# Kernel tuning notes

Hardware: AMD Instinct MI355X
Metric: run time of the kernel (lower is better)

The kernel has to match this reference:

```python
import jax, jax.numpy as jnp
import numpy as np


def setup_inputs() -> dict:
    key = jax.random.key(0)
    k1, k2, k3 = jax.random.split(key, 3)
    bs, chart_len, H = 256, 1024, 256
    num_steps, start_index = 512, 512
    chart = jax.random.normal(k1, (bs, chart_len, 2 * H), dtype=jnp.float32)
    operations = jax.random.randint(k2, (num_steps, bs, 2), 0, start_index, dtype=jnp.int64)
    U = jax.random.normal(k3, (5 * H, 2 * H), dtype=jnp.float32) * 0.05
    b = jnp.zeros((5 * H,), dtype=jnp.float32)
    return {"chart": chart, "operations": operations, "start_index": start_index, "U": U, "b": b}


def reference(chart, operations, start_index, U, b):
    H = U.shape[0] // 5
    bs = chart.shape[0]
    batch_idx = jnp.arange(bs)
    num_steps = operations.shape[0]

    def step_fn(ch, xs):
        step, ops = xs
        left = ch[batch_idx, ops[:, 0]]   # [bs, 2H]
        right = ch[batch_idx, ops[:, 1]]  # [bs, 2H]
        ccL, ccR = left[:, :H], right[:, :H]
        hh = jnp.concatenate([left[:, H:], right[:, H:]], axis=-1)  # [bs, 2H]
        preact = hh @ U.T + b  # [bs, 5H]
        i = jax.nn.sigmoid(preact[:, :H])
        fL = jax.nn.sigmoid(preact[:, H:2 * H])
        fR = jax.nn.sigmoid(preact[:, 2 * H:3 * H])
        o = jax.nn.sigmoid(preact[:, 3 * H:4 * H])
        u = jnp.tanh(preact[:, 4 * H:5 * H])
        c = fL * ccL + fR * ccR + i * u
        h = o * jnp.tanh(c)
        ch = ch.at[:, start_index + step, :].set(jnp.concatenate([c, h], axis=-1))
        return ch, None

    chart, _ = jax.lax.scan(step_fn, chart, (jnp.arange(num_steps), operations))
    return chart
```

## Files before the change

kernel.cpp:

```cpp
#include <hip/hip_runtime.h>
#include <hip/hip_bf16.h>

#define H_     256
#define TWOH_  512
#define CL_    1024
#define BS_    256
#define START_ 512

typedef float  f32x16   __attribute__((ext_vector_type(16)));
typedef short  short8_t __attribute__((ext_vector_type(8)));
typedef short  short4_t __attribute__((ext_vector_type(4)));
typedef __bf16 bf16x8   __attribute__((ext_vector_type(8)));

static __device__ __forceinline__ unsigned short f2bf(float x) {
  __hip_bfloat16 h = __float2bfloat16(x);
  return __builtin_bit_cast(unsigned short, h);
}

static __device__ __forceinline__ void gload16(const void* g, void* l) {
  __builtin_amdgcn_global_load_lds(
      (const __attribute__((address_space(1))) void*)g,
      (__attribute__((address_space(3))) void*)l, 16, 0, 0);
}

#define SCHED0() __builtin_amdgcn_sched_barrier(0)

__global__ void uconv_kernel(const float* __restrict__ U,
                             unsigned short* __restrict__ ub) {
  int tid = blockIdx.x * 256 + threadIdx.x;
  if (tid >= 1280 * 512) return;
  int n = tid >> 9, k = tid & 511;
  int g = n >> 8, j = n & 255;
  int jc = j >> 6, c = (g << 6) + (j & 63);
  ub[((jc * 320 + c) << 9) + k] = f2bf(U[tid]);
}

__global__ void hbconv_kernel(const float* __restrict__ chart,
                              unsigned short* __restrict__ hb) {
  size_t t = (size_t)blockIdx.x * 256 + threadIdx.x;
  size_t row = t >> 5;
  int    kc  = (int)(t & 31) * 8;
  size_t i = row >> 9, pos = row & 511;
  const float* src = chart + (i * CL_ + pos) * TWOH_ + H_ + kc;
  float4 f0 = *(const float4*)(src);
  float4 f1 = *(const float4*)(src + 4);
  short8_t v;
  v[0] = (short)f2bf(f0.x); v[1] = (short)f2bf(f0.y);
  v[2] = (short)f2bf(f0.z); v[3] = (short)f2bf(f0.w);
  v[4] = (short)f2bf(f1.x); v[5] = (short)f2bf(f1.y);
  v[6] = (short)f2bf(f1.z); v[7] = (short)f2bf(f1.w);
  *(short8_t*)(hb + row * H_ + kc) = v;
}

__global__ void copy_kernel(const float4* __restrict__ src,
                            float4* __restrict__ dst) {
  long long tid = (long long)blockIdx.x * blockDim.x + threadIdx.x;
  const long long total = 16777216LL;
  for (long long e = tid; e < total; e += (long long)gridDim.x * blockDim.x) {
    long long i   = e >> 16;
    long long rem = e & 65535;
    long long off = (i << 17) + rem;
    dst[off] = src[off];
  }
}

__global__ __launch_bounds__(256, 2) void chart3_kernel(
    const float* __restrict__ chart,
    const int* __restrict__ ops,
    const unsigned short* __restrict__ ub,
    const unsigned short* __restrict__ hb,
    const float* __restrict__ bias,
    float* __restrict__ out)
{
  __shared__ unsigned short As[2][128 * 32];
  __shared__ unsigned short Bs[2][320 * 32];
  __shared__ int opsl[256];

  const int tid = threadIdx.x;
  const int bx  = blockIdx.x;
  const int q5  = bx / 5;
  const int r5  = bx - q5 * 5;

  if (r5 == 4) {
    const float4* src = (const float4*)chart;
    float4* dst = (float4*)out;
    const long long base = (long long)q5 * 16384 + tid;
    #pragma unroll 4
    for (int it = 0; it < 64; ++it) {
      long long e   = base + it * 256;
      long long i   = e >> 16;
      long long rem = e & 65535;
      long long off = (i << 17) + rem;
      dst[off] = src[off];
    }
    return;
  }

  const int lane = tid & 63, wid = tid >> 6;
  const int l31 = lane & 31, lhi = lane >> 5;
  const int wm = wid & 1, wn = wid >> 1;
  const int s = q5 >> 1, ibase = (q5 & 1) * 128, jc = r5;

  opsl[tid] = ops[(s * BS_ + ibase) * 2 + tid];

  int rA[2], opAL[2], opAR[2], csA[2];
  #pragma unroll
  for (int q = 0; q < 2; ++q) {
    rA[q]   = (wid * 2 + q) * 16 + (lane >> 2);
    opAL[q] = ops[(s * BS_ + ibase + rA[q]) * 2];
    opAR[q] = ops[(s * BS_ + ibase + rA[q]) * 2 + 1];
    csA[q]  = (((lane & 3) ^ ((rA[q] >> 1) & 3))) * 8;
  }
  int rB[5], csB[5];
  #pragma unroll
  for (int p = 0; p < 5; ++p) {
    rB[p]  = (wid * 5 + p) * 16 + (lane >> 2);
    csB[p] = (((lane & 3) ^ ((rB[p] >> 1) & 3))) * 8;
  }
  const size_t ub_base = ((size_t)jc * 320) << 9;

  f32x16 acc0[5], acc1[5];
  #pragma unroll
  for (int g = 0; g < 5; ++g)
    #pragma unroll
    for (int q = 0; q < 16; ++q) { acc0[g][q] = 0.f; acc1[g][q] = 0.f; }

#define STAGE(BUF, KT) do {                                                     \
    const int  kt_   = (KT);                                                    \
    const bool left_ = kt_ < 8;                                                 \
    const int  koff_ = left_ ? kt_ * 32 : kt_ * 32 - 256;                       \
    _Pragma("unroll")                                                           \
    for (int q = 0; q < 2; ++q) {                                               \
      int op_ = left_ ? opAL[q] : opAR[q];                                      \
      const unsigned short* g_ =                                                \
          hb + ((size_t)(ibase + rA[q]) * 512 + op_) * 256 + koff_ + csA[q];    \
      gload16(g_, &As[BUF][(wid * 2 + q) * 512]);                               \
    }                                                                           \
    _Pragma("unroll")                                                           \
    for (int p = 0; p < 5; ++p) {                                               \
      const unsigned short* g_ =                                                \
          ub + ub_base + ((size_t)rB[p] << 9) + kt_ * 32 + csB[p];              \
      gload16(g_, &Bs[BUF][(wid * 5 + p) * 512]);                               \
    }                                                                           \
  } while (0)

  const int sw   = (l31 >> 1) & 3;
  const int aro0 = (wm * 64 + l31) * 32;
  const int aro1 = (wm * 64 + 32 + l31) * 32;
  const int bro  = (wn * 32 + l31) * 32;

#define COMPUTE(BUF) do {                                                       \
    _Pragma("unroll")                                                           \
    for (int ks = 0; ks < 2; ++ks) {                                            \
      const int ce = ((ks * 2 + lhi) ^ sw) * 8;                                 \
      bf16x8 a0 = __builtin_bit_cast(bf16x8,                                    \
          *(const short8_t*)&As[BUF][aro0 + ce]);                               \
      bf16x8 a1 = __builtin_bit_cast(bf16x8,                                    \
          *(const short8_t*)&As[BUF][aro1 + ce]);                               \
      _Pragma("unroll")                                                         \
      for (int g = 0; g < 5; ++g) {                                             \
        bf16x8 b = __builtin_bit_cast(bf16x8,                                   \
            *(const short8_t*)&Bs[BUF][bro + g * 2048 + ce]);                   \
        acc0[g] = __builtin_amdgcn_mfma_f32_32x32x16_bf16(a0, b, acc0[g],0,0,0);\
        acc1[g] = __builtin_amdgcn_mfma_f32_32x32x16_bf16(a1, b, acc1[g],0,0,0);\
      }                                                                         \
    }                                                                           \
  } while (0)

#define PHASE(BUF, KT, DOSTAGE) do {                                            \
    asm volatile("s_waitcnt vmcnt(7)" ::: "memory");                            \
    __builtin_amdgcn_s_barrier();                                               \
    SCHED0();                                                                   \
    COMPUTE(BUF);                                                               \
    SCHED0();                                                                   \
    __builtin_amdgcn_s_barrier();                                               \
    SCHED0();                                                                   \
    if (DOSTAGE) { STAGE(BUF, (KT) + 2); SCHED0(); }                            \
  } while (0)

  STAGE(0, 0); SCHED0();
  STAGE(1, 1); SCHED0();

  for (int kt = 0; kt < 14; kt += 2) {
    PHASE(0, kt,     true);
    PHASE(1, kt + 1, true);
  }
  PHASE(0, 14, false);
  asm volatile("s_waitcnt vmcnt(0)" ::: "memory");
  __builtin_amdgcn_s_barrier();
  SCHED0();
  COMPUTE(1);

#undef PHASE
#undef COMPUTE
#undef STAGE

  const int jlane = jc * 64 + wn * 32 + l31;
  float bg[5];
  #pragma unroll
  for (int g = 0; g < 5; ++g) bg[g] = bias[g * H_ + jlane];

#define EPI(ACC, M) do {                                                        \
    _Pragma("unroll")                                                           \
    for (int q = 0; q < 16; ++q) {                                              \
      const int row_ = wm * 64 + (M) * 32 + (q & 3) + 8 * (q >> 2) + 4 * lhi;   \
      const int i_   = ibase + row_;                                            \
      const int opL_ = opsl[2 * row_], opR_ = opsl[2 * row_ + 1];               \
      const float ccL_ = chart[((size_t)i_ * CL_ + opL_) * TWOH_ + jlane];      \
      const float ccR_ = chart[((size_t)i_ * CL_ + opR_) * TWOH_ + jlane];      \
      float pi_  = (ACC)[0][q] + bg[0];                                         \
      float pfL_ = (ACC)[1][q] + bg[1];                                         \
      float pfR_ = (ACC)[2][q] + bg[2];                                         \
      float po_  = (ACC)[3][q] + bg[3];                                         \
      float pu_  = (ACC)[4][q] + bg[4];                                         \
      float gi_  = 1.f / (1.f + __expf(-pi_));                                  \
      float gfL_ = 1.f / (1.f + __expf(-pfL_));                                 \
      float gfR_ = 1.f / (1.f + __expf(-pfR_));                                 \
      float go_  = 1.f / (1.f + __expf(-po_));                                  \
      float eu_  = __expf(2.f * pu_);                                           \
      float gu_  = 1.f - 2.f / (eu_ + 1.f);                                     \
      float c_   = gfL_ * ccL_ + gfR_ * ccR_ + gi_ * gu_;                       \
      float ec_  = __expf(2.f * c_);                                            \
      float th_  = 1.f - 2.f / (ec_ + 1.f);                                     \
      float h_   = go_ * th_;                                                   \
      float* orow_ = out + ((size_t)i_ * CL_ + START_ + s) * TWOH_;             \
      orow_[jlane]      = c_;                                                   \
      orow_[H_ + jlane] = h_;                                                   \
    }                                                                           \
  } while (0)

  EPI(acc0, 0);
  EPI(acc1, 1);
#undef EPI
}

__global__ __launch_bounds__(256, 2) void chart1_kernel(
    const float* __restrict__ chart,
    const int* __restrict__ ops,
    const float* __restrict__ U,
    const float* __restrict__ bias,
    float* __restrict__ out)
{
  __shared__ unsigned short As[64 * 72];
  __shared__ unsigned short Bs[320 * 72];
  __shared__ int opsl[128];

  const int tid = threadIdx.x, lane = tid & 63, wid = tid >> 6;
  const int wm = wid & 1, wn = wid >> 1;
  const int bx = blockIdx.x, jc = blockIdx.y;
  const int s = bx >> 2, ibase = (bx & 3) * 64, j0 = jc * 64;

  if (tid < 128) opsl[tid] = ops[(s * BS_ + ibase) * 2 + tid];
  __syncthreads();

  const int arow = tid >> 2, aqc = tid & 3;
  const int opL_s = opsl[2 * arow], opR_s = opsl[2 * arow + 1];
  const long long abase_i = (long long)(ibase + arow) * CL_;

  f32x16 acc[5];
  #pragma unroll
  for (int g = 0; g < 5; ++g)
    #pragma unroll
    for (int q = 0; q < 16; ++q) acc[g][q] = 0.0f;

  const int a_off  = (wm * 32 + (lane & 31)) * 72 + 8 * (lane >> 5);
  const int b_off0 = (wn * 32 + (lane & 31)) * 72 + 8 * (lane >> 5);

  for (int kt = 0; kt < 8; ++kt) {
    const int k0 = kt * 64;
    {
      const int op   = (k0 < 256) ? opL_s : opR_s;
      const int col0 = ((k0 < 256) ? 256 + k0 : k0) + aqc * 16;
      const float* src = chart + (abase_i + op) * TWOH_ + col0;
      float4 f0 = *(const float4*)(src + 0);
      float4 f1 = *(const float4*)(src + 4);
      float4 f2 = *(const float4*)(src + 8);
      float4 f3 = *(const float4*)(src + 12);
      short8_t v0, v1;
      v0[0] = (short)f2bf(f0.x); v0[1] = (short)f2bf(f0.y);
      v0[2] = (short)f2bf(f0.z); v0[3] = (short)f2bf(f0.w);
      v0[4] = (short)f2bf(f1.x); v0[5] = (short)f2bf(f1.y);
      v0[6] = (short)f2bf(f1.z); v0[7] = (short)f2bf(f1.w);
      v1[0] = (short)f2bf(f2.x); v1[1] = (short)f2bf(f2.y);
      v1[2] = (short)f2bf(f2.z); v1[3] = (short)f2bf(f2.w);
      v1[4] = (short)f2bf(f3.x); v1[5] = (short)f2bf(f3.y);
      v1[6] = (short)f2bf(f3.z); v1[7] = (short)f2bf(f3.w);
      *(short8_t*)&As[arow * 72 + aqc * 16]     = v0;
      *(short8_t*)&As[arow * 72 + aqc * 16 + 8] = v1;
    }
    #pragma unroll
    for (int cc = 0; cc < 20; ++cc) {
      int chunk = cc * 256 + tid;
      int c  = chunk >> 4;
      int ko = (chunk & 15) * 4;
      int n  = ((c >> 6) << 8) + j0 + (c & 63);
      float4 f = *(const float4*)(U + (long long)n * 512 + k0 + ko);
      short4_t v;
      v[0] = (short)f2bf(f.x); v[1] = (short)f2bf(f.y);
      v[2] = (short)f2bf(f.z); v[3] = (short)f2bf(f.w);
      *(short4_t*)&Bs[c * 72 + ko] = v;
    }
    __syncthreads();

    #pragma unroll
    for (int ks = 0; ks < 4; ++ks) {
      bf16x8 a = __builtin_bit_cast(bf16x8, *(const short8_t*)&As[a_off + ks * 16]);
      #pragma unroll
      for (int g = 0; g < 5; ++g) {
        bf16x8 b = __builtin_bit_cast(bf16x8,
            *(const short8_t*)&Bs[b_off0 + g * 64 * 72 + ks * 16]);
        acc[g] = __builtin_amdgcn_mfma_f32_32x32x16_bf16(a, b, acc[g], 0, 0, 0);
      }
    }
    __syncthreads();
  }

  const int jlane = j0 + wn * 32 + (lane & 31);
  float bg[5];
  #pragma unroll
  for (int g = 0; g < 5; ++g) bg[g] = bias[g * H_ + jlane];

  #pragma unroll
  for (int q = 0; q < 16; ++q) {
    int rl  = wm * 32 + (q & 3) + 8 * (q >> 2) + 4 * (lane >> 5);
    int i   = ibase + rl;
    int opL = opsl[2 * rl], opR = opsl[2 * rl + 1];
    float ccL = chart[((long long)i * CL_ + opL) * TWOH_ + jlane];
    float ccR = chart[((long long)i * CL_ + opR) * TWOH_ + jlane];
    float pi  = acc[0][q] + bg[0];
    float pfL = acc[1][q] + bg[1];
    float pfR = acc[2][q] + bg[2];
    float po  = acc[3][q] + bg[3];
    float pu  = acc[4][q] + bg[4];
    float gi  = 1.f / (1.f + __expf(-pi));
    float gfL = 1.f / (1.f + __expf(-pfL));
    float gfR = 1.f / (1.f + __expf(-pfR));
    float go  = 1.f / (1.f + __expf(-po));
    float eu  = __expf(2.f * pu);
    float gu  = 1.f - 2.f / (eu + 1.f);
    float c   = gfL * ccL + gfR * ccR + gi * gu;
    float ec  = __expf(2.f * c);
    float th  = 1.f - 2.f / (ec + 1.f);
    float h   = go * th;
    float* orow = out + ((long long)i * CL_ + START_ + s) * TWOH_;
    orow[jlane]      = c;
    orow[H_ + jlane] = h;
  }
}

extern "C" void kernel_launch(void* const* d_in, const int* in_sizes, int n_in,
                              void* d_out, int out_size, void* d_ws, size_t ws_size,
                              hipStream_t stream) {
  const float* chart = (const float*)d_in[0];
  const int*   ops   = (const int*)d_in[1];
  const float* U     = (const float*)d_in[3];
  const float* bias  = (const float*)d_in[4];
  float* out = (float*)d_out;

  const size_t HB_OFF   = (size_t)2 << 20;
  const size_t HB_BYTES = (size_t)256 * 512 * 256 * 2;

  if (ws_size >= HB_OFF + HB_BYTES) {
    unsigned short* ub = (unsigned short*)d_ws;
    unsigned short* hb = (unsigned short*)((char*)d_ws + HB_OFF);
    uconv_kernel<<<2560, 256, 0, stream>>>(U, ub);
    hbconv_kernel<<<16384, 256, 0, stream>>>(chart, hb);
    chart3_kernel<<<5120, 256, 0, stream>>>(chart, ops, ub, hb, bias, out);
  } else {
    copy_kernel<<<4096, 256, 0, stream>>>((const float4*)chart, (float4*)out);
    chart1_kernel<<<dim3(2048, 4), 256, 0, stream>>>(chart, ops, U, bias, out);
  }
}
```

Measured before the change: 438.9 us.

## Fuse chart copy into bf16 conversion and enlarge GEMM tile to 256 rows

The chart copy now happens inside the bf16 h-conversion pass, so the first half of each sequence is read once instead of twice, and the copy blocks are removed from the main kernel. The main kernel now uses 512-thread blocks that cover all 256 batch rows and 64 columns per gate, with a K-step of 64, a swizzled LDS layout, block-index remapping and raised wave priority during MFMA. The larger tile cuts how often B is reloaded and halves the number of loop phases. The cost is more LDS and registers per block, which may limit occupancy.

```diff
diff --git a/kernel.cpp b/kernel.cpp
--- a/kernel.cpp
+++ b/kernel.cpp
@@ -35,21 +35,26 @@
   ub[((jc * 320 + c) << 9) + k] = f2bf(U[tid]);
 }
 
-__global__ void hbconv_kernel(const float* __restrict__ chart,
+__global__ void hbcopy_kernel(const float4* __restrict__ chart4,
+                              float4* __restrict__ out4,
                               unsigned short* __restrict__ hb) {
-  size_t t = (size_t)blockIdx.x * 256 + threadIdx.x;
-  size_t row = t >> 5;
-  int    kc  = (int)(t & 31) * 8;
-  size_t i = row >> 9, pos = row & 511;
-  const float* src = chart + (i * CL_ + pos) * TWOH_ + H_ + kc;
-  float4 f0 = *(const float4*)(src);
-  float4 f1 = *(const float4*)(src + 4);
-  short8_t v;
-  v[0] = (short)f2bf(f0.x); v[1] = (short)f2bf(f0.y);
-  v[2] = (short)f2bf(f0.z); v[3] = (short)f2bf(f0.w);
-  v[4] = (short)f2bf(f1.x); v[5] = (short)f2bf(f1.y);
-  v[6] = (short)f2bf(f1.z); v[7] = (short)f2bf(f1.w);
-  *(short8_t*)(hb + row * H_ + kc) = v;
+  const long long total = 16777216LL;
+  long long tid = (long long)blockIdx.x * blockDim.x + threadIdx.x;
+  for (long long e = tid; e < total; e += (long long)gridDim.x * blockDim.x) {
+    long long i   = e >> 16;
+    long long rem = e & 65535;
+    long long off = (i << 17) + rem;
+    float4 f = chart4[off];
+    out4[off] = f;
+    int col4 = (int)(rem & 127);
+    if (col4 >= 64) {
+      long long pos = rem >> 7;
+      short4_t v;
+      v[0] = (short)f2bf(f.x); v[1] = (short)f2bf(f.y);
+      v[2] = (short)f2bf(f.z); v[3] = (short)f2bf(f.w);
+      *(short4_t*)(hb + ((i * 512 + pos) * 256 + (long long)(col4 - 64) * 4)) = v;
+    }
+  }
 }
 
 __global__ void copy_kernel(const float4* __restrict__ src,
@@ -64,7 +69,7 @@
   }
 }
 
-__global__ __launch_bounds__(256, 2) void chart3_kernel(
+__global__ __launch_bounds__(512, 2) void chart4_kernel(
     const float* __restrict__ chart,
     const int* __restrict__ ops,
     const unsigned short* __restrict__ ub,
@@ -72,106 +77,90 @@
     const float* __restrict__ bias,
     float* __restrict__ out)
 {
-  __shared__ unsigned short As[2][128 * 32];
-  __shared__ unsigned short Bs[2][320 * 32];
-  __shared__ int opsl[256];
-
-  const int tid = threadIdx.x;
-  const int bx  = blockIdx.x;
-  const int q5  = bx / 5;
-  const int r5  = bx - q5 * 5;
-
-  if (r5 == 4) {
-    const float4* src = (const float4*)chart;
-    float4* dst = (float4*)out;
-    const long long base = (long long)q5 * 16384 + tid;
-    #pragma unroll 4
-    for (int it = 0; it < 64; ++it) {
-      long long e   = base + it * 256;
-      long long i   = e >> 16;
-      long long rem = e & 65535;
-      long long off = (i << 17) + rem;
-      dst[off] = src[off];
-    }
-    return;
-  }
-
-  const int lane = tid & 63, wid = tid >> 6;
+  __shared__ unsigned short As[2][256 * 64];
+  __shared__ unsigned short Bs[2][320 * 64];
+  __shared__ int opsl[512];
+
+  const int tid = threadIdx.x, lane = tid & 63, wid = tid >> 6;
   const int l31 = lane & 31, lhi = lane >> 5;
-  const int wm = wid & 1, wn = wid >> 1;
-  const int s = q5 >> 1, ibase = (q5 & 1) * 128, jc = r5;
-
-  opsl[tid] = ops[(s * BS_ + ibase) * 2 + tid];
-
-  int rA[2], opAL[2], opAR[2], csA[2];
-  #pragma unroll
-  for (int q = 0; q < 2; ++q) {
-    rA[q]   = (wid * 2 + q) * 16 + (lane >> 2);
-    opAL[q] = ops[(s * BS_ + ibase + rA[q]) * 2];
-    opAR[q] = ops[(s * BS_ + ibase + rA[q]) * 2 + 1];
-    csA[q]  = (((lane & 3) ^ ((rA[q] >> 1) & 3))) * 8;
-  }
-  int rB[5], csB[5];
+  const int wm = wid >> 1, wn = wid & 1;
+
+  const int bx = blockIdx.x;
+  const int g  = (bx & 7) * 256 + (bx >> 3);
+  const int s  = g >> 2, jc = g & 3;
+
+  opsl[tid] = ops[s * 512 + tid];
+  __syncthreads();
+
+  const int arow   = tid >> 3;
+  const int slotA  = tid & 7;
+  const int chunkA = slotA ^ (arow & 7);
+  int opL256[4], opR256[4];
+  const unsigned short* hbA[4];
+  #pragma unroll
+  for (int p = 0; p < 4; ++p) {
+    int row = arow + p * 64;
+    opL256[p] = opsl[2 * row] * 256;
+    opR256[p] = opsl[2 * row + 1] * 256;
+    hbA[p] = hb + ((size_t)row * 512) * 256 + chunkA * 8;
+  }
+  const unsigned short* ubB[5];
   #pragma unroll
   for (int p = 0; p < 5; ++p) {
-    rB[p]  = (wid * 5 + p) * 16 + (lane >> 2);
-    csB[p] = (((lane & 3) ^ ((rB[p] >> 1) & 3))) * 8;
-  }
-  const size_t ub_base = ((size_t)jc * 320) << 9;
+    int row = arow + p * 64;
+    ubB[p] = ub + (((size_t)(jc * 320 + row)) << 9) + chunkA * 8;
+  }
 
   f32x16 acc0[5], acc1[5];
   #pragma unroll
-  for (int g = 0; g < 5; ++g)
+  for (int gg = 0; gg < 5; ++gg)
     #pragma unroll
-    for (int q = 0; q < 16; ++q) { acc0[g][q] = 0.f; acc1[g][q] = 0.f; }
+    for (int q = 0; q < 16; ++q) { acc0[gg][q] = 0.f; acc1[gg][q] = 0.f; }
 
 #define STAGE(BUF, KT) do {                                                     \
-    const int  kt_   = (KT);                                                    \
-    const bool left_ = kt_ < 8;                                                 \
-    const int  koff_ = left_ ? kt_ * 32 : kt_ * 32 - 256;                       \
+    const int koff_ = ((KT) < 4) ? (KT) * 64 : (KT) * 64 - 256;                 \
     _Pragma("unroll")                                                           \
-    for (int q = 0; q < 2; ++q) {                                               \
-      int op_ = left_ ? opAL[q] : opAR[q];                                      \
+    for (int p = 0; p < 4; ++p) {                                               \
       const unsigned short* g_ =                                                \
-          hb + ((size_t)(ibase + rA[q]) * 512 + op_) * 256 + koff_ + csA[q];    \
-      gload16(g_, &As[BUF][(wid * 2 + q) * 512]);                               \
+          hbA[p] + (((KT) < 4) ? opL256[p] : opR256[p]) + koff_;                \
+      gload16(g_, &As[BUF][(p * 512 + tid) * 8]);                               \
     }                                                                           \
     _Pragma("unroll")                                                           \
     for (int p = 0; p < 5; ++p) {                                               \
-      const unsigned short* g_ =                                                \
-          ub + ub_base + ((size_t)rB[p] << 9) + kt_ * 32 + csB[p];              \
-      gload16(g_, &Bs[BUF][(wid * 5 + p) * 512]);                               \
+      gload16(ubB[p] + (KT) * 64, &Bs[BUF][(p * 512 + tid) * 8]);               \
     }                                                                           \
   } while (0)
 
-  const int sw   = (l31 >> 1) & 3;
-  const int aro0 = (wm * 64 + l31) * 32;
-  const int aro1 = (wm * 64 + 32 + l31) * 32;
-  const int bro  = (wn * 32 + l31) * 32;
+  const int sw7  = l31 & 7;
+  const int aro0 = (wm * 64 + l31) * 64;
+  const int aro1 = aro0 + 32 * 64;
+  const int bro  = (wn * 32 + l31) * 64;
 
 #define COMPUTE(BUF) do {                                                       \
     _Pragma("unroll")                                                           \
-    for (int ks = 0; ks < 2; ++ks) {                                            \
-      const int ce = ((ks * 2 + lhi) ^ sw) * 8;                                 \
+    for (int ks = 0; ks < 4; ++ks) {                                            \
+      const int ce = ((ks * 2 + lhi) ^ sw7) * 8;                                \
       bf16x8 a0 = __builtin_bit_cast(bf16x8,                                    \
           *(const short8_t*)&As[BUF][aro0 + ce]);                               \
       bf16x8 a1 = __builtin_bit_cast(bf16x8,                                    \
           *(const short8_t*)&As[BUF][aro1 + ce]);                               \
       _Pragma("unroll")                                                         \
-      for (int g = 0; g < 5; ++g) {                                             \
+      for (int gg = 0; gg < 5; ++gg) {                                          \
         bf16x8 b = __builtin_bit_cast(bf16x8,                                   \
-            *(const short8_t*)&Bs[BUF][bro + g * 2048 + ce]);                   \
-        acc0[g] = __builtin_amdgcn_mfma_f32_32x32x16_bf16(a0, b, acc0[g],0,0,0);\
-        acc1[g] = __builtin_amdgcn_mfma_f32_32x32x16_bf16(a1, b, acc1[g],0,0,0);\
+            *(const short8_t*)&Bs[BUF][bro + gg * 4096 + ce]);                  \
+        acc0[gg] = __builtin_amdgcn_mfma_f32_32x32x16_bf16(a0,b,acc0[gg],0,0,0);\
+        acc1[gg] = __builtin_amdgcn_mfma_f32_32x32x16_bf16(a1,b,acc1[gg],0,0,0);\
       }                                                                         \
     }                                                                           \
   } while (0)
 
 #define PHASE(BUF, KT, DOSTAGE) do {                                            \
-    asm volatile("s_waitcnt vmcnt(7)" ::: "memory");                            \
+    asm volatile("s_waitcnt vmcnt(9)" ::: "memory");                            \
     __builtin_amdgcn_s_barrier();                                               \
     SCHED0();                                                                   \
+    __builtin_amdgcn_s_setprio(1);                                              \
     COMPUTE(BUF);                                                               \
+    __builtin_amdgcn_s_setprio(0);                                              \
     SCHED0();                                                                   \
     __builtin_amdgcn_s_barrier();                                               \
     SCHED0();                                                                   \
@@ -181,11 +170,12 @@
   STAGE(0, 0); SCHED0();
   STAGE(1, 1); SCHED0();
 
-  for (int kt = 0; kt < 14; kt += 2) {
+  #pragma unroll
+  for (int kt = 0; kt < 6; kt += 2) {
     PHASE(0, kt,     true);
     PHASE(1, kt + 1, true);
   }
-  PHASE(0, 14, false);
+  PHASE(0, 6, false);
   asm volatile("s_waitcnt vmcnt(0)" ::: "memory");
   __builtin_amdgcn_s_barrier();
   SCHED0();
@@ -198,14 +188,13 @@
   const int jlane = jc * 64 + wn * 32 + l31;
   float bg[5];
   #pragma unroll
-  for (int g = 0; g < 5; ++g) bg[g] = bias[g * H_ + jlane];
-
-#define EPI(ACC, M) do {                                                        \
+  for (int gg = 0; gg < 5; ++gg) bg[gg] = bias[gg * H_ + jlane];
+
+#define EPI(ACC, MF) do {                                                       \
     _Pragma("unroll")                                                           \
     for (int q = 0; q < 16; ++q) {                                              \
-      const int row_ = wm * 64 + (M) * 32 + (q & 3) + 8 * (q >> 2) + 4 * lhi;   \
-      const int i_   = ibase + row_;                                            \
-      const int opL_ = opsl[2 * row_], opR_ = opsl[2 * row_ + 1];               \
+      const int i_   = wm * 64 + (MF) * 32 + (q & 3) + 8 * (q >> 2) + 4 * lhi;  \
+      const int opL_ = opsl[2 * i_], opR_ = opsl[2 * i_ + 1];                   \
       const float ccL_ = chart[((size_t)i_ * CL_ + opL_) * TWOH_ + jlane];      \
       const float ccR_ = chart[((size_t)i_ * CL_ + opR_) * TWOH_ + jlane];      \
       float pi_  = (ACC)[0][q] + bg[0];                                         \
@@ -364,8 +353,8 @@
     unsigned short* ub = (unsigned short*)d_ws;
     unsigned short* hb = (unsigned short*)((char*)d_ws + HB_OFF);
     uconv_kernel<<<2560, 256, 0, stream>>>(U, ub);
-    hbconv_kernel<<<16384, 256, 0, stream>>>(chart, hb);
-    chart3_kernel<<<5120, 256, 0, stream>>>(chart, ops, ub, hb, bias, out);
+    hbcopy_kernel<<<4096, 256, 0, stream>>>((const float4*)chart, (float4*)out, hb);
+    chart4_kernel<<<2048, 512, 0, stream>>>(chart, ops, ub, hb, bias, out);
   } else {
     copy_kernel<<<4096, 256, 0, stream>>>((const float4*)chart, (float4*)out);
     chart1_kernel<<<dim3(2048, 4), 256, 0, stream>>>(chart, ops, U, bias, out);
```

Result: faster. 407.6 us (-7.1%).
